# Performance work log

Measured on AMD Instinct MI355X. Metric: run time of the kernel, lower is better.

## Reference

```python
import jax, jax.numpy as jnp
import numpy as np

N_NODES = 100_000
N_EDGES = 1_600_000
F_DIM = 32


def setup_inputs() -> dict:
    key = jax.random.key(0)
    k1, k2, k3 = jax.random.split(key, 3)
    x = jax.random.normal(k1, (N_NODES, F_DIM), dtype=jnp.float32)
    edge_index = jax.random.randint(k2, (2, N_EDGES), 0, N_NODES, dtype=jnp.int64)
    edge_weight = jax.random.uniform(k3, (N_EDGES,), dtype=jnp.float32)
    w_mp = jnp.array([0.5], dtype=jnp.float32)  # learned scalar parameter
    return {"x": x, "edge_index": edge_index, "edge_weight": edge_weight, "w_mp": w_mp}


def reference(x, edge_index, edge_weight, w_mp):
    # message: ea = w_mp * x[src] * edge_weight  (shape [E, F])
    # aggregate: sum messages into target nodes (aggr='add', source_to_target)
    src = edge_index[0]
    dst = edge_index[1]
    ea = (w_mp * x[src]) * edge_weight[:, None]          # [E, F]
    out = jax.ops.segment_sum(ea, dst, num_segments=x.shape[0])  # [N, F]
    return out
```

## Files before the change

### kernel.cpp

```cpp
#include <hip/hip_runtime.h>


constexpr int N_NODES = 100000;
constexpr int N_EDGES = 1600000;
constexpr int F_DIM   = 32;

constexpr int NPB_C = 256;
constexpr int NB_C  = (N_NODES + NPB_C - 1) / NPB_C;
constexpr int CAP_C = 4608;

constexpr int BIN_THREADS = 512;
constexpr int BIN_EPT     = 16;
constexpr int BIN_CHUNK   = BIN_THREADS * BIN_EPT;
constexpr int BIN_BLOCKS  = (N_EDGES + BIN_CHUNK - 1) / BIN_CHUNK;

constexpr int SUBS  = 4;
constexpr int NPB_F = NPB_C / SUBS;
constexpr int MCAP  = 1344;
constexpr int AGG_THREADS = 512;
constexpr int RPT = (MCAP + AGG_THREADS - 1) / AGG_THREADS;

constexpr size_t WS_CURSOR  = 0;
constexpr size_t WS_RECORDS = 4096;
constexpr size_t WS_NEEDED  = WS_RECORDS + (size_t)NB_C * CAP_C * 8;

__global__ __launch_bounds__(256) void init_cursors(int* __restrict__ gcursor)
{
    int i = blockIdx.x * 256 + threadIdx.x;
    if (i < NB_C) gcursor[i] = i * CAP_C;
}

__global__ __launch_bounds__(BIN_THREADS) void bin_edges(
    const int* __restrict__ src, const int* __restrict__ dst,
    const float* __restrict__ ew, const float* __restrict__ w_mp,
    int* __restrict__ gcursor, uint2* __restrict__ records)
{
    __shared__ int lhist[NB_C];
    __shared__ int lbase[NB_C];
    if (threadIdx.x < NB_C) lhist[threadIdx.x] = 0;
    __syncthreads();

    const float w = w_mp[0];
    const int base_e = blockIdx.x * BIN_CHUNK;
    int   bkt[BIN_EPT];
    uint2 rec[BIN_EPT];

    #pragma unroll
    for (int i = 0; i < BIN_EPT; ++i) {
        int e = base_e + threadIdx.x + i * BIN_THREADS;
        bkt[i] = -1;
        if (e < N_EDGES) {
            int d = dst[e];
            int b = d >> 8;
            bkt[i] = b;
            rec[i].x = __float_as_uint(w * ew[e]);
            rec[i].y = (unsigned)src[e] | ((unsigned)(d & 255) << 24);
            atomicAdd(&lhist[b], 1);
        }
    }
    __syncthreads();

    if (threadIdx.x < NB_C) {
        int c = lhist[threadIdx.x];
        lbase[threadIdx.x] = c ? atomicAdd(&gcursor[threadIdx.x], c) : 0;
        lhist[threadIdx.x] = 0;
    }
    __syncthreads();

    #pragma unroll
    for (int i = 0; i < BIN_EPT; ++i) {
        int b = bkt[i];
        if (b >= 0) {
            int pos = lbase[b] + atomicAdd(&lhist[b], 1);
            if (pos < (b + 1) * CAP_C)
                records[pos] = rec[i];
        }
    }
}

__global__ __launch_bounds__(AGG_THREADS) void sort_gather(
    const int*   __restrict__ gcursor,
    const uint2* __restrict__ records,
    const float* __restrict__ x,
    float*       __restrict__ out)
{
    __shared__ uint2 mine[MCAP];
    __shared__ uint2 sorted[MCAP];
    __shared__ int   hist[NPB_F];
    __shared__ int   offs[NPB_F + 1];
    __shared__ int   cursor[NPB_F];
    __shared__ int   mcount;

    const int coarse   = blockIdx.x >> 2;
    const unsigned sub = blockIdx.x & 3;
    const int t        = threadIdx.x;
    const int lane     = t & 63;

    if (t < NPB_F) hist[t] = 0;
    if (t == 0) mcount = 0;
    __syncthreads();

    const int rbase = coarse * CAP_C;
    const int cnt   = min(gcursor[coarse] - rbase, CAP_C);
    for (int j = t; j < cnt; j += AGG_THREADS) {
        uint2 r = records[rbase + j];
        bool match = (r.y >> 30) == sub;
        unsigned long long m = __ballot(match);
        if (m) {
            int lead = __ffsll(m) - 1;
            int base = 0;
            if (lane == lead) base = atomicAdd(&mcount, __popcll(m));
            base = __shfl(base, lead, 64);
            if (match) {
                int slot = base + __popcll(m & ((1ull << lane) - 1));
                if (slot < MCAP) mine[slot] = r;
            }
        }
    }
    __syncthreads();

    const int M = min(mcount, MCAP);
    uint2 rec[RPT];
    #pragma unroll
    for (int i = 0; i < RPT; ++i) {
        int j = t + i * AGG_THREADS;
        rec[i].y = 0xFFFFFFFFu;
        if (j < M) {
            rec[i] = mine[j];
            atomicAdd(&hist[(rec[i].y >> 24) & 63], 1);
        }
    }
    __syncthreads();

    if (t < 64) {
        int v   = hist[t];
        int inc = v;
        #pragma unroll
        for (int d = 1; d < 64; d <<= 1) {
            int o = __shfl_up(inc, d, 64);
            if (t >= d) inc += o;
        }
        offs[t + 1] = inc;
        if (t == 0) offs[0] = 0;
        cursor[t] = inc - v;
    }
    __syncthreads();

    #pragma unroll
    for (int i = 0; i < RPT; ++i) {
        if (rec[i].y != 0xFFFFFFFFu) {
            int slot = atomicAdd(&cursor[(rec[i].y >> 24) & 63], 1);
            sorted[slot] = rec[i];
        }
    }
    __syncthreads();

    const int node  = t >> 3;
    const int q     = (t & 7) * 4;
    const int gnode = coarse * NPB_C + (int)sub * NPB_F + node;
    if (gnode >= N_NODES) return;

    int j  = offs[node];
    int je = offs[node + 1];
    float4 acc = make_float4(0.f, 0.f, 0.f, 0.f);

    for (; j + 4 <= je; j += 4) {
        uint2 r0 = sorted[j + 0];
        uint2 r1 = sorted[j + 1];
        uint2 r2 = sorted[j + 2];
        uint2 r3 = sorted[j + 3];
        const float4 v0 = *reinterpret_cast<const float4*>(
            x + (size_t)(r0.y & 0xFFFFFFu) * F_DIM + q);
        const float4 v1 = *reinterpret_cast<const float4*>(
            x + (size_t)(r1.y & 0xFFFFFFu) * F_DIM + q);
        const float4 v2 = *reinterpret_cast<const float4*>(
            x + (size_t)(r2.y & 0xFFFFFFu) * F_DIM + q);
        const float4 v3 = *reinterpret_cast<const float4*>(
            x + (size_t)(r3.y & 0xFFFFFFu) * F_DIM + q);
        float c0 = __uint_as_float(r0.x), c1 = __uint_as_float(r1.x);
        float c2 = __uint_as_float(r2.x), c3 = __uint_as_float(r3.x);
        acc.x += c0 * v0.x + c1 * v1.x + c2 * v2.x + c3 * v3.x;
        acc.y += c0 * v0.y + c1 * v1.y + c2 * v2.y + c3 * v3.y;
        acc.z += c0 * v0.z + c1 * v1.z + c2 * v2.z + c3 * v3.z;
        acc.w += c0 * v0.w + c1 * v1.w + c2 * v2.w + c3 * v3.w;
    }
    for (; j < je; ++j) {
        uint2 r = sorted[j];
        float c = __uint_as_float(r.x);
        const float4 v = *reinterpret_cast<const float4*>(
            x + (size_t)(r.y & 0xFFFFFFu) * F_DIM + q);
        acc.x += c * v.x;
        acc.y += c * v.y;
        acc.z += c * v.z;
        acc.w += c * v.w;
    }
    *reinterpret_cast<float4*>(out + (size_t)gnode * F_DIM + q) = acc;
}

__global__ __launch_bounds__(256) void gnn_scatter_atomic(
    const float* __restrict__ x, const int* __restrict__ src,
    const int* __restrict__ dst, const float* __restrict__ ew,
    const float* __restrict__ w_mp, float* __restrict__ out)
{
    const float w = w_mp[0];
    int gid = blockIdx.x * blockDim.x + threadIdx.x;
    int e = gid >> 3;
    int qq = (gid & 7) * 4;
    if (e >= N_EDGES) return;
    int s = src[e];
    int d = dst[e];
    float c = w * ew[e];
    const float4 xv = *reinterpret_cast<const float4*>(x + (size_t)s * F_DIM + qq);
    float* op = out + (size_t)d * F_DIM + qq;
    atomicAdd(op + 0, c * xv.x);
    atomicAdd(op + 1, c * xv.y);
    atomicAdd(op + 2, c * xv.z);
    atomicAdd(op + 3, c * xv.w);
}

extern "C" void kernel_launch(void* const* d_in, const int* in_sizes, int n_in,
                              void* d_out, int out_size, void* d_ws, size_t ws_size,
                              hipStream_t stream) {
    const float* x    = (const float*)d_in[0];
    const int*   ei   = (const int*)d_in[1];
    const float* ew   = (const float*)d_in[2];
    const float* w_mp = (const float*)d_in[3];
    float* out = (float*)d_out;

    const int* src = ei;
    const int* dst = ei + N_EDGES;

    if (ws_size < WS_NEEDED) {
        hipMemsetAsync(d_out, 0, (size_t)out_size * sizeof(float), stream);
        int total = N_EDGES * 8;
        gnn_scatter_atomic<<<(total + 255) / 256, 256, 0, stream>>>(
            x, src, dst, ew, w_mp, out);
        return;
    }

    char* ws = (char*)d_ws;
    int*   gcursor = (int*)(ws + WS_CURSOR);
    uint2* records = (uint2*)(ws + WS_RECORDS);

    init_cursors<<<(NB_C + 255) / 256, 256, 0, stream>>>(gcursor);
    bin_edges<<<BIN_BLOCKS, BIN_THREADS, 0, stream>>>(src, dst, ew, w_mp,
                                                      gcursor, records);
    sort_gather<<<NB_C * SUBS, AGG_THREADS, 0, stream>>>(gcursor, records, x, out);
}
```

Baseline: 128.9 us.

## Restructure sort_gather into two-pass counting sort with half-coarse sub-buckets

Cursors now count from zero, set by a memset instead of an init kernel, and records are indexed as bucket*CAP plus offset. sort_gather splits each coarse bucket into 2 sub-blocks of 128 nodes instead of 4. It histograms directly from global records and scatters in a second pass, dropping the intermediate shared 'mine' staging buffer and the ballot compaction. Each thread now accumulates 8 features with two float4 loads, and bin_edges handles 8 edges per thread. The cost is reading each bucket's records from global memory twice per sub-block, though half as many blocks read each bucket.

```diff
diff --git a/kernel.cpp b/kernel.cpp
--- a/kernel.cpp
+++ b/kernel.cpp
@@ -10,25 +10,18 @@
 constexpr int CAP_C = 4608;
 
 constexpr int BIN_THREADS = 512;
-constexpr int BIN_EPT     = 16;
+constexpr int BIN_EPT     = 8;
 constexpr int BIN_CHUNK   = BIN_THREADS * BIN_EPT;
 constexpr int BIN_BLOCKS  = (N_EDGES + BIN_CHUNK - 1) / BIN_CHUNK;
 
-constexpr int SUBS  = 4;
+constexpr int SUBS  = 2;
 constexpr int NPB_F = NPB_C / SUBS;
-constexpr int MCAP  = 1344;
-constexpr int AGG_THREADS = 512;
-constexpr int RPT = (MCAP + AGG_THREADS - 1) / AGG_THREADS;
+constexpr int MCAP  = 2560;
+constexpr int SG_THREADS = 512;
 
 constexpr size_t WS_CURSOR  = 0;
 constexpr size_t WS_RECORDS = 4096;
 constexpr size_t WS_NEEDED  = WS_RECORDS + (size_t)NB_C * CAP_C * 8;
-
-__global__ __launch_bounds__(256) void init_cursors(int* __restrict__ gcursor)
-{
-    int i = blockIdx.x * 256 + threadIdx.x;
-    if (i < NB_C) gcursor[i] = i * CAP_C;
-}
 
 __global__ __launch_bounds__(BIN_THREADS) void bin_edges(
     const int* __restrict__ src, const int* __restrict__ dst,
@@ -71,130 +64,126 @@
     for (int i = 0; i < BIN_EPT; ++i) {
         int b = bkt[i];
         if (b >= 0) {
-            int pos = lbase[b] + atomicAdd(&lhist[b], 1);
-            if (pos < (b + 1) * CAP_C)
-                records[pos] = rec[i];
-        }
-    }
-}
-
-__global__ __launch_bounds__(AGG_THREADS) void sort_gather(
+            int ofs = lbase[b] + atomicAdd(&lhist[b], 1);
+            if (ofs < CAP_C)
+                records[b * CAP_C + ofs] = rec[i];
+        }
+    }
+}
+
+__global__ __launch_bounds__(SG_THREADS) void sort_gather(
     const int*   __restrict__ gcursor,
     const uint2* __restrict__ records,
     const float* __restrict__ x,
     float*       __restrict__ out)
 {
-    __shared__ uint2 mine[MCAP];
     __shared__ uint2 sorted[MCAP];
     __shared__ int   hist[NPB_F];
     __shared__ int   offs[NPB_F + 1];
     __shared__ int   cursor[NPB_F];
-    __shared__ int   mcount;
-
-    const int coarse   = blockIdx.x >> 2;
-    const unsigned sub = blockIdx.x & 3;
+
+    const int coarse   = blockIdx.x >> 1;
+    const unsigned sub = blockIdx.x & 1;
     const int t        = threadIdx.x;
-    const int lane     = t & 63;
 
     if (t < NPB_F) hist[t] = 0;
-    if (t == 0) mcount = 0;
     __syncthreads();
 
     const int rbase = coarse * CAP_C;
-    const int cnt   = min(gcursor[coarse] - rbase, CAP_C);
-    for (int j = t; j < cnt; j += AGG_THREADS) {
-        uint2 r = records[rbase + j];
-        bool match = (r.y >> 30) == sub;
-        unsigned long long m = __ballot(match);
-        if (m) {
-            int lead = __ffsll(m) - 1;
-            int base = 0;
-            if (lane == lead) base = atomicAdd(&mcount, __popcll(m));
-            base = __shfl(base, lead, 64);
-            if (match) {
-                int slot = base + __popcll(m & ((1ull << lane) - 1));
-                if (slot < MCAP) mine[slot] = r;
-            }
-        }
-    }
-    __syncthreads();
-
-    const int M = min(mcount, MCAP);
-    uint2 rec[RPT];
-    #pragma unroll
-    for (int i = 0; i < RPT; ++i) {
-        int j = t + i * AGG_THREADS;
-        rec[i].y = 0xFFFFFFFFu;
-        if (j < M) {
-            rec[i] = mine[j];
-            atomicAdd(&hist[(rec[i].y >> 24) & 63], 1);
-        }
+    const int cnt   = min(gcursor[coarse], CAP_C);
+
+    for (int j = t; j < cnt; j += SG_THREADS) {
+        unsigned ry = records[rbase + j].y;
+        if ((ry >> 31) == sub)
+            atomicAdd(&hist[(ry >> 24) & 127], 1);
     }
     __syncthreads();
 
     if (t < 64) {
-        int v   = hist[t];
-        int inc = v;
+        int v0  = hist[t];
+        int inc = v0;
         #pragma unroll
         for (int d = 1; d < 64; d <<= 1) {
             int o = __shfl_up(inc, d, 64);
             if (t >= d) inc += o;
         }
         offs[t + 1] = inc;
+        cursor[t]   = inc - v0;
+        int tot0 = __shfl(inc, 63, 64);
+        int v1   = hist[64 + t];
+        int inc1 = v1;
+        #pragma unroll
+        for (int d = 1; d < 64; d <<= 1) {
+            int o = __shfl_up(inc1, d, 64);
+            if (t >= d) inc1 += o;
+        }
+        offs[64 + t + 1] = tot0 + inc1;
+        cursor[64 + t]   = tot0 + inc1 - v1;
         if (t == 0) offs[0] = 0;
-        cursor[t] = inc - v;
-    }
-    __syncthreads();
-
-    #pragma unroll
-    for (int i = 0; i < RPT; ++i) {
-        if (rec[i].y != 0xFFFFFFFFu) {
-            int slot = atomicAdd(&cursor[(rec[i].y >> 24) & 63], 1);
-            sorted[slot] = rec[i];
-        }
-    }
-    __syncthreads();
-
-    const int node  = t >> 3;
-    const int q     = (t & 7) * 4;
+    }
+    __syncthreads();
+
+    for (int j = t; j < cnt; j += SG_THREADS) {
+        uint2 r = records[rbase + j];
+        if ((r.y >> 31) == sub) {
+            int slot = atomicAdd(&cursor[(r.y >> 24) & 127], 1);
+            if (slot < MCAP) sorted[slot] = r;
+        }
+    }
+    __syncthreads();
+
+    const int node  = t >> 2;
+    const int h     = (t & 3) * 8;
     const int gnode = coarse * NPB_C + (int)sub * NPB_F + node;
     if (gnode >= N_NODES) return;
 
-    int j  = offs[node];
-    int je = offs[node + 1];
-    float4 acc = make_float4(0.f, 0.f, 0.f, 0.f);
+    int j  = min(offs[node], MCAP);
+    int je = min(offs[node + 1], MCAP);
+    float4 accA = make_float4(0.f, 0.f, 0.f, 0.f);
+    float4 accB = make_float4(0.f, 0.f, 0.f, 0.f);
 
     for (; j + 4 <= je; j += 4) {
         uint2 r0 = sorted[j + 0];
         uint2 r1 = sorted[j + 1];
         uint2 r2 = sorted[j + 2];
         uint2 r3 = sorted[j + 3];
-        const float4 v0 = *reinterpret_cast<const float4*>(
-            x + (size_t)(r0.y & 0xFFFFFFu) * F_DIM + q);
-        const float4 v1 = *reinterpret_cast<const float4*>(
-            x + (size_t)(r1.y & 0xFFFFFFu) * F_DIM + q);
-        const float4 v2 = *reinterpret_cast<const float4*>(
-            x + (size_t)(r2.y & 0xFFFFFFu) * F_DIM + q);
-        const float4 v3 = *reinterpret_cast<const float4*>(
-            x + (size_t)(r3.y & 0xFFFFFFu) * F_DIM + q);
+        const float* p0 = x + (size_t)(r0.y & 0xFFFFFFu) * F_DIM + h;
+        const float* p1 = x + (size_t)(r1.y & 0xFFFFFFu) * F_DIM + h;
+        const float* p2 = x + (size_t)(r2.y & 0xFFFFFFu) * F_DIM + h;
+        const float* p3 = x + (size_t)(r3.y & 0xFFFFFFu) * F_DIM + h;
+        float4 a0 = *reinterpret_cast<const float4*>(p0);
+        float4 b0 = *reinterpret_cast<const float4*>(p0 + 4);
+        float4 a1 = *reinterpret_cast<const float4*>(p1);
+        float4 b1 = *reinterpret_cast<const float4*>(p1 + 4);
+        float4 a2 = *reinterpret_cast<const float4*>(p2);
+        float4 b2 = *reinterpret_cast<const float4*>(p2 + 4);
+        float4 a3 = *reinterpret_cast<const float4*>(p3);
+        float4 b3 = *reinterpret_cast<const float4*>(p3 + 4);
         float c0 = __uint_as_float(r0.x), c1 = __uint_as_float(r1.x);
         float c2 = __uint_as_float(r2.x), c3 = __uint_as_float(r3.x);
-        acc.x += c0 * v0.x + c1 * v1.x + c2 * v2.x + c3 * v3.x;
-        acc.y += c0 * v0.y + c1 * v1.y + c2 * v2.y + c3 * v3.y;
-        acc.z += c0 * v0.z + c1 * v1.z + c2 * v2.z + c3 * v3.z;
-        acc.w += c0 * v0.w + c1 * v1.w + c2 * v2.w + c3 * v3.w;
+        accA.x += c0 * a0.x + c1 * a1.x + c2 * a2.x + c3 * a3.x;
+        accA.y += c0 * a0.y + c1 * a1.y + c2 * a2.y + c3 * a3.y;
+        accA.z += c0 * a0.z + c1 * a1.z + c2 * a2.z + c3 * a3.z;
+        accA.w += c0 * a0.w + c1 * a1.w + c2 * a2.w + c3 * a3.w;
+        accB.x += c0 * b0.x + c1 * b1.x + c2 * b2.x + c3 * b3.x;
+        accB.y += c0 * b0.y + c1 * b1.y + c2 * b2.y + c3 * b3.y;
+        accB.z += c0 * b0.z + c1 * b1.z + c2 * b2.z + c3 * b3.z;
+        accB.w += c0 * b0.w + c1 * b1.w + c2 * b2.w + c3 * b3.w;
     }
     for (; j < je; ++j) {
         uint2 r = sorted[j];
         float c = __uint_as_float(r.x);
-        const float4 v = *reinterpret_cast<const float4*>(
-            x + (size_t)(r.y & 0xFFFFFFu) * F_DIM + q);
-        acc.x += c * v.x;
-        acc.y += c * v.y;
-        acc.z += c * v.z;
-        acc.w += c * v.w;
-    }
-    *reinterpret_cast<float4*>(out + (size_t)gnode * F_DIM + q) = acc;
+        const float* p = x + (size_t)(r.y & 0xFFFFFFu) * F_DIM + h;
+        float4 a = *reinterpret_cast<const float4*>(p);
+        float4 bb = *reinterpret_cast<const float4*>(p + 4);
+        accA.x += c * a.x;  accA.y += c * a.y;
+        accA.z += c * a.z;  accA.w += c * a.w;
+        accB.x += c * bb.x; accB.y += c * bb.y;
+        accB.z += c * bb.z; accB.w += c * bb.w;
+    }
+    float4* o = reinterpret_cast<float4*>(out + (size_t)gnode * F_DIM + h);
+    o[0] = accA;
+    o[1] = accB;
 }
 
 __global__ __launch_bounds__(256) void gnn_scatter_atomic(
@@ -242,8 +231,8 @@
     int*   gcursor = (int*)(ws + WS_CURSOR);
     uint2* records = (uint2*)(ws + WS_RECORDS);
 
-    init_cursors<<<(NB_C + 255) / 256, 256, 0, stream>>>(gcursor);
+    hipMemsetAsync(gcursor, 0, NB_C * sizeof(int), stream);
     bin_edges<<<BIN_BLOCKS, BIN_THREADS, 0, stream>>>(src, dst, ew, w_mp,
                                                       gcursor, records);
-    sort_gather<<<NB_C * SUBS, AGG_THREADS, 0, stream>>>(gcursor, records, x, out);
-}
+    sort_gather<<<NB_C * SUBS, SG_THREADS, 0, stream>>>(gcursor, records, x, out);
+}
```

Result: no change. 131.5 us (+2.0%).
